# Performance work log

Hardware: AMD Instinct MI355X
Metric: run time of the kernel (lower is better)

## Reference

```python
import jax, jax.numpy as jnp
import numpy as np

N_NODES = 50000
N_EDGES = 800000
D_FEAT = 96
HIDDEN = 96
AVG_DEG = 16.0


def setup_inputs() -> dict:
    key = jax.random.key(0)
    k1, k2, k3, k4, k5 = jax.random.split(key, 5)
    x = jax.random.normal(k1, (N_NODES, D_FEAT), dtype=jnp.float32)
    row = jax.random.randint(k2, (N_EDGES,), 0, N_NODES)
    col = jax.random.randint(k3, (N_EDGES,), 0, N_NODES)
    edge_index = jnp.stack([row, col]).astype(jnp.int32)  # [2, E]
    # normalized adjacency values ~ 1/degree scale
    edge_weight = jax.random.uniform(k4, (N_EDGES,), dtype=jnp.float32) / AVG_DEG
    # init_w: small normal + identity (random=False path)
    W = 0.1 * jax.random.normal(k5, (D_FEAT, HIDDEN), dtype=jnp.float32) + jnp.eye(D_FEAT, HIDDEN, dtype=jnp.float32)
    b = jnp.zeros((HIDDEN,), dtype=jnp.float32)
    return {"x": x, "W": W, "b": b, "edge_index": edge_index, "edge_weight": edge_weight}


def reference(x, W, b, edge_index, edge_weight):
    # dense projection + bias
    h = x @ W + b  # [N, H]
    # sparse adj matmul: out[i] = sum_e w_e * h[col_e] for row_e == i
    row, col = edge_index[0], edge_index[1]
    msgs = edge_weight[:, None] * h[col]  # [E, H]
    pre_nonlinearity = jax.ops.segment_sum(msgs, row, num_segments=N_NODES)  # [N, H]
    # inference path: no dropout (training=None)
    output = jax.nn.elu(pre_nonlinearity)
    return (pre_nonlinearity, output)
```

## Files before the change

kernel.cpp:

```cpp
#include <hip/hip_runtime.h>


#define D 96
#define CG 24
#define BSHIFT 5
#define BROWS 32
#define CAP 768
#define CPAD 16
#define EB_CHUNK 3200
#define NBKT_MAX 1600
#define GR 64
#define XPITCH 25

typedef unsigned long long u64;
typedef unsigned short u16;
typedef unsigned int u32;

__device__ __forceinline__ u16 f2bf(float f) {
  const u32 u = __float_as_uint(f);
  return (u16)((u + 0x7FFFu + ((u >> 16) & 1u)) >> 16);
}
__device__ __forceinline__ float bf2f(u16 s) {
  return __uint_as_float(((u32)s) << 16);
}

struct ushort4_t { u16 x, y, z, w; };

__global__ __launch_bounds__(256) void init_bcur_kernel(int* __restrict__ bcur, int nbkt) {
  const int b = blockIdx.x * 256 + threadIdx.x;
  if (b < nbkt) bcur[b * CPAD] = b * CAP;
}

union FusedSmem {
  float4 sX[GR * XPITCH];
  struct { int cnt[NBKT_MAX]; int cur[NBKT_MAX]; } bz;
};

__global__ __launch_bounds__(256) void fused_gemm_bucketize(
    const float* __restrict__ x, const float4* __restrict__ W4,
    const float* __restrict__ bias, u16* __restrict__ h16, int n_nodes,
    const int* __restrict__ rows, const int* __restrict__ cols,
    const float* __restrict__ ew, int* __restrict__ bcur,
    u64* __restrict__ tmp, int n_edges, int nbkt, int bb) {
  __shared__ FusedSmem sm;
  const int tid = threadIdx.x;

  if ((int)blockIdx.x < bb) {
    for (int i = tid; i < NBKT_MAX; i += 256) sm.bz.cnt[i] = 0;
    __syncthreads();
    const int e0 = blockIdx.x * EB_CHUNK;
    const int e1 = min(e0 + EB_CHUNK, n_edges);
    for (int e = e0 + tid; e < e1; e += 256)
      atomicAdd(&sm.bz.cnt[rows[e] >> BSHIFT], 1);
    __syncthreads();
    for (int b = tid; b < nbkt; b += 256) {
      const int c = sm.bz.cnt[b];
      sm.bz.cur[b] = (c > 0) ? atomicAdd(&bcur[b * CPAD], c) : 0;
    }
    __syncthreads();
    for (int e = e0 + tid; e < e1; e += 256) {
      const int r = rows[e];
      const int b = r >> BSHIFT;
      const u64 u = ((u64)__float_as_uint(ew[e]) << 32) |
                    ((u64)(r & (BROWS - 1)) << 20) | (u64)(unsigned)cols[e];
      const int pos = atomicAdd(&sm.bz.cur[b], 1);
      if (pos < (b + 1) * CAP) tmp[pos] = u;
    }
  } else {
    const int row0 = ((int)blockIdx.x - bb) * GR;
    for (int i = tid; i < GR * CG; i += 256) {
      const int r = i / CG, c = i % CG;
      float4 v = make_float4(0.f, 0.f, 0.f, 0.f);
      const int gr = row0 + r;
      if (gr < n_nodes) v = ((const float4*)x)[(size_t)gr * CG + c];
      sm.sX[r * XPITCH + c] = v;
    }
    __syncthreads();
    if (tid < 192) {
      const int cg = tid >> 3;
      const int rq = tid & 7;
      float4 acc[8];
      const float4 bv = ((const float4*)bias)[cg];
#pragma unroll
      for (int j = 0; j < 8; ++j) acc[j] = bv;

#define FMA4(A, XS, WV) \
  A.x = fmaf(XS, WV.x, A.x); A.y = fmaf(XS, WV.y, A.y); \
  A.z = fmaf(XS, WV.z, A.z); A.w = fmaf(XS, WV.w, A.w);

      for (int kb = 0; kb < 24; ++kb) {
        const float4 w0 = W4[(kb * 4 + 0) * CG + cg];
        const float4 w1 = W4[(kb * 4 + 1) * CG + cg];
        const float4 w2 = W4[(kb * 4 + 2) * CG + cg];
        const float4 w3 = W4[(kb * 4 + 3) * CG + cg];
#pragma unroll
        for (int j = 0; j < 8; ++j) {
          const float4 xv = sm.sX[(rq + 8 * j) * XPITCH + kb];
          FMA4(acc[j], xv.x, w0);
          FMA4(acc[j], xv.y, w1);
          FMA4(acc[j], xv.z, w2);
          FMA4(acc[j], xv.w, w3);
        }
      }
#pragma unroll
      for (int j = 0; j < 8; ++j) {
        const int r = row0 + rq + 8 * j;
        if (r < n_nodes) {
          ushort4_t o;
          o.x = f2bf(acc[j].x); o.y = f2bf(acc[j].y);
          o.z = f2bf(acc[j].z); o.w = f2bf(acc[j].w);
          ((ushort4_t*)h16)[(size_t)r * CG + cg] = o;
        }
      }
    }
  }
}

__global__ __launch_bounds__(256) void bucket_gather_kernel(
    const int* __restrict__ bcur, const u64* __restrict__ tmp,
    const u16* __restrict__ h16, float* __restrict__ pre,
    float* __restrict__ out, int n_nodes) {
  __shared__ u64 raw[CAP];
  __shared__ u64 se[CAP];
  __shared__ int cnt[BROWS];
  __shared__ int off[BROWS + 1];
  __shared__ int cur[BROWS];
  const int tid = threadIdx.x;
  const int b = blockIdx.x;
  if (tid < BROWS) cnt[tid] = 0;
  __syncthreads();

  const int base = b * CAP;
  int count = bcur[b * CPAD] - base;
  if (count > CAP) count = CAP;

  for (int k = tid; k < count; k += 256) {
    const u64 u = tmp[base + k];
    raw[k] = u;
    atomicAdd(&cnt[(int)((u >> 20) & (BROWS - 1))], 1);
  }
  __syncthreads();

  if (tid < BROWS) off[tid + 1] = cnt[tid];
  if (tid == 0) off[0] = 0;
  __syncthreads();
  for (int d = 1; d <= BROWS; d <<= 1) {
    int v = 0;
    if (tid <= BROWS && tid >= d) v = off[tid - d];
    __syncthreads();
    if (tid <= BROWS) off[tid] += v;
    __syncthreads();
  }
  if (tid < BROWS) cur[tid] = off[tid];
  __syncthreads();

  for (int k = tid; k < count; k += 256) {
    const u64 u = raw[k];
    const int rl = (int)((u >> 20) & (BROWS - 1));
    se[atomicAdd(&cur[rl], 1)] = u;
  }
  __syncthreads();

  const int g = tid >> 5;
  const int lane = tid & 31;
  const int row0 = b * BROWS;
#pragma unroll
  for (int j = 0; j < 4; ++j) {
    const int r = g * 4 + j;
    const int row = row0 + r;
    const int s = off[r], e = off[r + 1];
    float a0 = 0.f, a1 = 0.f, a2 = 0.f;
    int k = s;
    for (; k + 3 < e; k += 4) {
      const u64 u0 = se[k], u1 = se[k + 1], u2 = se[k + 2], u3 = se[k + 3];
      const u16* h0 = h16 + (size_t)(u0 & 0xFFFFF) * D;
      const u16* h1 = h16 + (size_t)(u1 & 0xFFFFF) * D;
      const u16* h2 = h16 + (size_t)(u2 & 0xFFFFF) * D;
      const u16* h3 = h16 + (size_t)(u3 & 0xFFFFF) * D;
      const float w0 = __uint_as_float((u32)(u0 >> 32));
      const float w1 = __uint_as_float((u32)(u1 >> 32));
      const float w2 = __uint_as_float((u32)(u2 >> 32));
      const float w3 = __uint_as_float((u32)(u3 >> 32));
      const float p00 = bf2f(h0[lane]), p01 = bf2f(h0[lane + 32]), p02 = bf2f(h0[lane + 64]);
      const float p10 = bf2f(h1[lane]), p11 = bf2f(h1[lane + 32]), p12 = bf2f(h1[lane + 64]);
      const float p20 = bf2f(h2[lane]), p21 = bf2f(h2[lane + 32]), p22 = bf2f(h2[lane + 64]);
      const float p30 = bf2f(h3[lane]), p31 = bf2f(h3[lane + 32]), p32 = bf2f(h3[lane + 64]);
      a0 = fmaf(w0, p00, a0); a1 = fmaf(w0, p01, a1); a2 = fmaf(w0, p02, a2);
      a0 = fmaf(w1, p10, a0); a1 = fmaf(w1, p11, a1); a2 = fmaf(w1, p12, a2);
      a0 = fmaf(w2, p20, a0); a1 = fmaf(w2, p21, a1); a2 = fmaf(w2, p22, a2);
      a0 = fmaf(w3, p30, a0); a1 = fmaf(w3, p31, a1); a2 = fmaf(w3, p32, a2);
    }
    for (; k < e; ++k) {
      const u64 u = se[k];
      const u16* hr = h16 + (size_t)(u & 0xFFFFF) * D;
      const float w = __uint_as_float((u32)(u >> 32));
      a0 = fmaf(w, bf2f(hr[lane]), a0);
      a1 = fmaf(w, bf2f(hr[lane + 32]), a1);
      a2 = fmaf(w, bf2f(hr[lane + 64]), a2);
    }
    if (row < n_nodes) {
      float* pr = pre + (size_t)row * D;
      float* orow = out + (size_t)row * D;
      pr[lane] = a0; pr[lane + 32] = a1; pr[lane + 64] = a2;
      orow[lane]      = a0 > 0.f ? a0 : (__expf(a0) - 1.f);
      orow[lane + 32] = a1 > 0.f ? a1 : (__expf(a1) - 1.f);
      orow[lane + 64] = a2 > 0.f ? a2 : (__expf(a2) - 1.f);
    }
  }
}

extern "C" void kernel_launch(void* const* d_in, const int* in_sizes, int n_in,
                              void* d_out, int out_size, void* d_ws, size_t ws_size,
                              hipStream_t stream) {
  const float* x  = (const float*)d_in[0];
  const float* W  = (const float*)d_in[1];
  const float* b  = (const float*)d_in[2];
  const int*   ei = (const int*)d_in[3];
  const float* ew = (const float*)d_in[4];

  const int n_nodes = in_sizes[0] / D;
  const int n_edges = in_sizes[4];
  const int* rows = ei;
  const int* cols = ei + n_edges;

  float* pre  = (float*)d_out;
  float* outp = pre + (size_t)n_nodes * D;

  const int nbkt = (n_nodes + BROWS - 1) / BROWS;

  char* ws = (char*)d_ws;
  u16*  h16  = (u16*)ws;   ws += (size_t)n_nodes * D * sizeof(u16);
  int*  bcur = (int*)ws;   ws += (size_t)nbkt * CPAD * sizeof(int);
  u64*  tmp  = (u64*)ws;

  init_bcur_kernel<<<(nbkt + 255) / 256, 256, 0, stream>>>(bcur, nbkt);

  const int gb = (n_nodes + GR - 1) / GR;
  const int bb = (n_edges + EB_CHUNK - 1) / EB_CHUNK;
  fused_gemm_bucketize<<<gb + bb, 256, 0, stream>>>(
      x, (const float4*)W, b, h16, n_nodes,
      rows, cols, ew, bcur, tmp, n_edges, nbkt, bb);

  bucket_gather_kernel<<<nbkt, 256, 0, stream>>>(bcur, tmp, h16, pre, outp, n_nodes);
}
```

Before: 153.8 us.

## Use split-bf16 MFMA for projection GEMM and cache row ids in LDS

Replaces the scalar FP32 FMA projection with bf16 MFMA 16x16x32 instructions, using a hi/lo split of x and W (three MFMAs per tile) to keep near-FP32 accuracy. W is converted and transposed into LDS per block. The bucketize pass now caches row indices in shared memory so rows are not read from global twice, and the bucket cursor init kernel is replaced by a memset with relative offsets. Each GEMM block redundantly converts all of W, which adds LDS traffic and per-block setup work.

Result: no change. 153.8 us (-0.0%).

```diff
diff --git a/kernel.cpp b/kernel.cpp
--- a/kernel.cpp
+++ b/kernel.cpp
@@ -2,7 +2,6 @@
 
 
 #define D 96
-#define CG 24
 #define BSHIFT 5
 #define BROWS 32
 #define CAP 768
@@ -10,12 +9,16 @@
 #define EB_CHUNK 3200
 #define NBKT_MAX 1600
 #define GR 64
-#define XPITCH 25
+#define KP 104
 
 typedef unsigned long long u64;
 typedef unsigned short u16;
 typedef unsigned int u32;
 
+typedef __attribute__((ext_vector_type(8))) __bf16 bf8_t;
+typedef __attribute__((ext_vector_type(8))) short s8_t;
+typedef __attribute__((ext_vector_type(4))) float f4_t;
+
 __device__ __forceinline__ u16 f2bf(float f) {
   const u32 u = __float_as_uint(f);
   return (u16)((u + 0x7FFFu + ((u >> 16) & 1u)) >> 16);
@@ -24,20 +27,18 @@
   return __uint_as_float(((u32)s) << 16);
 }
 
-struct ushort4_t { u16 x, y, z, w; };
-
-__global__ __launch_bounds__(256) void init_bcur_kernel(int* __restrict__ bcur, int nbkt) {
-  const int b = blockIdx.x * 256 + threadIdx.x;
-  if (b < nbkt) bcur[b * CPAD] = b * CAP;
-}
-
-union FusedSmem {
-  float4 sX[GR * XPITCH];
-  struct { int cnt[NBKT_MAX]; int cur[NBKT_MAX]; } bz;
+__device__ __forceinline__ f4_t mfma16(s8_t a, s8_t b, f4_t c) {
+  return __builtin_amdgcn_mfma_f32_16x16x32_bf16(
+      __builtin_bit_cast(bf8_t, a), __builtin_bit_cast(bf8_t, b), c, 0, 0, 0);
+}
+
+union __align__(16) FusedSmem {
+  struct { u16 hi[96 * KP]; u16 lo[96 * KP]; } w;
+  struct { int cnt[NBKT_MAX]; int cur[NBKT_MAX]; int rbuf[EB_CHUNK]; } bz;
 };
 
 __global__ __launch_bounds__(256) void fused_gemm_bucketize(
-    const float* __restrict__ x, const float4* __restrict__ W4,
+    const float* __restrict__ x, const float* __restrict__ W,
     const float* __restrict__ bias, u16* __restrict__ h16, int n_nodes,
     const int* __restrict__ rows, const int* __restrict__ cols,
     const float* __restrict__ ew, int* __restrict__ bcur,
@@ -50,8 +51,11 @@
     __syncthreads();
     const int e0 = blockIdx.x * EB_CHUNK;
     const int e1 = min(e0 + EB_CHUNK, n_edges);
-    for (int e = e0 + tid; e < e1; e += 256)
-      atomicAdd(&sm.bz.cnt[rows[e] >> BSHIFT], 1);
+    for (int e = e0 + tid; e < e1; e += 256) {
+      const int r = rows[e];
+      sm.bz.rbuf[e - e0] = r;
+      atomicAdd(&sm.bz.cnt[r >> BSHIFT], 1);
+    }
     __syncthreads();
     for (int b = tid; b < nbkt; b += 256) {
       const int c = sm.bz.cnt[b];
@@ -59,58 +63,73 @@
     }
     __syncthreads();
     for (int e = e0 + tid; e < e1; e += 256) {
-      const int r = rows[e];
+      const int r = sm.bz.rbuf[e - e0];
       const int b = r >> BSHIFT;
       const u64 u = ((u64)__float_as_uint(ew[e]) << 32) |
                     ((u64)(r & (BROWS - 1)) << 20) | (u64)(unsigned)cols[e];
       const int pos = atomicAdd(&sm.bz.cur[b], 1);
-      if (pos < (b + 1) * CAP) tmp[pos] = u;
+      if (pos < CAP) tmp[(size_t)b * CAP + pos] = u;
     }
   } else {
-    const int row0 = ((int)blockIdx.x - bb) * GR;
-    for (int i = tid; i < GR * CG; i += 256) {
-      const int r = i / CG, c = i % CG;
-      float4 v = make_float4(0.f, 0.f, 0.f, 0.f);
-      const int gr = row0 + r;
-      if (gr < n_nodes) v = ((const float4*)x)[(size_t)gr * CG + c];
-      sm.sX[r * XPITCH + c] = v;
-    }
-    __syncthreads();
-    if (tid < 192) {
-      const int cg = tid >> 3;
-      const int rq = tid & 7;
-      float4 acc[8];
-      const float4 bv = ((const float4*)bias)[cg];
-#pragma unroll
-      for (int j = 0; j < 8; ++j) acc[j] = bv;
-
-#define FMA4(A, XS, WV) \
-  A.x = fmaf(XS, WV.x, A.x); A.y = fmaf(XS, WV.y, A.y); \
-  A.z = fmaf(XS, WV.z, A.z); A.w = fmaf(XS, WV.w, A.w);
-
-      for (int kb = 0; kb < 24; ++kb) {
-        const float4 w0 = W4[(kb * 4 + 0) * CG + cg];
-        const float4 w1 = W4[(kb * 4 + 1) * CG + cg];
-        const float4 w2 = W4[(kb * 4 + 2) * CG + cg];
-        const float4 w3 = W4[(kb * 4 + 3) * CG + cg];
-#pragma unroll
-        for (int j = 0; j < 8; ++j) {
-          const float4 xv = sm.sX[(rq + 8 * j) * XPITCH + kb];
-          FMA4(acc[j], xv.x, w0);
-          FMA4(acc[j], xv.y, w1);
-          FMA4(acc[j], xv.z, w2);
-          FMA4(acc[j], xv.w, w3);
-        }
+    for (int e = tid; e < 96 * 96; e += 256) {
+      const int k = e / 96;
+      const int n = e - k * 96;
+      const float w = W[e];
+      const u16 hb = f2bf(w);
+      sm.w.hi[n * KP + k] = hb;
+      sm.w.lo[n * KP + k] = f2bf(w - bf2f(hb));
+    }
+    __syncthreads();
+
+    const int wid = tid >> 6;
+    const int lane = tid & 63;
+    const int l15 = lane & 15;
+    const int g = lane >> 4;
+    const int row0 = ((int)blockIdx.x - bb) * GR + wid * 16;
+
+    const int ra = min(row0 + l15, n_nodes - 1);
+    const float* xr = x + (size_t)ra * D;
+    s8_t ah[3], al[3];
+#pragma unroll
+    for (int kt = 0; kt < 3; ++kt) {
+      const float4 v0 = *(const float4*)(xr + kt * 32 + 8 * g);
+      const float4 v1 = *(const float4*)(xr + kt * 32 + 8 * g + 4);
+      const float vv[8] = {v0.x, v0.y, v0.z, v0.w, v1.x, v1.y, v1.z, v1.w};
+#pragma unroll
+      for (int j = 0; j < 8; ++j) {
+        const u16 hb = f2bf(vv[j]);
+        ah[kt][j] = (short)hb;
+        al[kt][j] = (short)f2bf(vv[j] - bf2f(hb));
       }
-#pragma unroll
-      for (int j = 0; j < 8; ++j) {
-        const int r = row0 + rq + 8 * j;
-        if (r < n_nodes) {
-          ushort4_t o;
-          o.x = f2bf(acc[j].x); o.y = f2bf(acc[j].y);
-          o.z = f2bf(acc[j].z); o.w = f2bf(acc[j].w);
-          ((ushort4_t*)h16)[(size_t)r * CG + cg] = o;
-        }
+    }
+
+    f4_t acc[6];
+#pragma unroll
+    for (int n = 0; n < 6; ++n) {
+      const float bv = bias[n * 16 + l15];
+      acc[n][0] = bv; acc[n][1] = bv; acc[n][2] = bv; acc[n][3] = bv;
+    }
+
+#pragma unroll
+    for (int kt = 0; kt < 3; ++kt) {
+#pragma unroll
+      for (int n = 0; n < 6; ++n) {
+        const int wo = (n * 16 + l15) * KP + kt * 32 + 8 * g;
+        const s8_t bh = *(const s8_t*)&sm.w.hi[wo];
+        const s8_t bl = *(const s8_t*)&sm.w.lo[wo];
+        acc[n] = mfma16(ah[kt], bh, acc[n]);
+        acc[n] = mfma16(al[kt], bh, acc[n]);
+        acc[n] = mfma16(ah[kt], bl, acc[n]);
+      }
+    }
+
+#pragma unroll
+    for (int n = 0; n < 6; ++n) {
+#pragma unroll
+      for (int r = 0; r < 4; ++r) {
+        const int row = row0 + 4 * g + r;
+        if (row < n_nodes)
+          h16[(size_t)row * D + n * 16 + l15] = f2bf(acc[n][r]);
       }
     }
   }
@@ -131,7 +150,7 @@
   __syncthreads();
 
   const int base = b * CAP;
-  int count = bcur[b * CPAD] - base;
+  int count = bcur[b * CPAD];
   if (count > CAP) count = CAP;
 
   for (int k = tid; k < count; k += 256) {
@@ -233,13 +252,12 @@
   int*  bcur = (int*)ws;   ws += (size_t)nbkt * CPAD * sizeof(int);
   u64*  tmp  = (u64*)ws;
 
-  init_bcur_kernel<<<(nbkt + 255) / 256, 256, 0, stream>>>(bcur, nbkt);
+  hipMemsetAsync(bcur, 0, (size_t)nbkt * CPAD * sizeof(int), stream);
 
   const int gb = (n_nodes + GR - 1) / GR;
   const int bb = (n_edges + EB_CHUNK - 1) / EB_CHUNK;
   fused_gemm_bucketize<<<gb + bb, 256, 0, stream>>>(
-      x, (const float4*)W, b, h16, n_nodes,
-      rows, cols, ew, bcur, tmp, n_edges, nbkt, bb);
+      x, W, b, h16, n_nodes, rows, cols, ew, bcur, tmp, n_edges, nbkt, bb);
 
   bucket_gather_kernel<<<nbkt, 256, 0, stream>>>(bcur, tmp, h16, pre, outp, n_nodes);
 }
```
